# Optimization experiments

Hardware: AMD Instinct MI355X
Metric: run time of the kernel (lower is better)

## Reference

```python
import jax, jax.numpy as jnp
import numpy as np

T, N, E, B = 6, 3200, 32000, 8
IN, G, TOK, H, NH = 128, 128, 512, 4, 8
HD = TOK // NH
NEG_SLOPE = 0.2  # PyG GATv2Conv default negative_slope
L_GAT, L_TF = 3, 2


def _ln(x, g, b, eps=1e-5):
    mu = x.mean(-1, keepdims=True)
    var = ((x - mu) ** 2).mean(-1, keepdims=True)
    return (x - mu) * jax.lax.rsqrt(var + eps) * g + b


def setup_inputs() -> dict:
    key = jax.random.key(0)
    ks = iter(jax.random.split(key, 64))
    nrm = lambda shape, s=0.05: (jax.random.normal(next(ks), shape) * s).astype(jnp.float32)
    return dict(
        x=jax.random.normal(next(ks), (T, N, IN), jnp.float32),
        edge_index=jax.random.randint(next(ks), (T, 2, E), 0, N, dtype=jnp.int32),
        edge_attr=jax.random.normal(next(ks), (T, E, 2), jnp.float32),
        batch=jnp.sort(jax.random.randint(next(ks), (N,), 0, B, dtype=jnp.int32)),
        proj_w=nrm((IN, G)), proj_b=jnp.zeros((G,), jnp.float32),
        gat_wl=nrm((L_GAT, G, H * G)), gat_bl=jnp.zeros((L_GAT, H * G), jnp.float32),
        gat_wr=nrm((L_GAT, G, H * G)), gat_br=jnp.zeros((L_GAT, H * G), jnp.float32),
        gat_we=nrm((L_GAT, 2, H * G)),
        gat_att=nrm((L_GAT, H, G)),
        gat_bias=jnp.zeros((L_GAT, G), jnp.float32),
        ln_g=jnp.ones((L_GAT, G), jnp.float32), ln_b=jnp.zeros((L_GAT, G), jnp.float32),
        n2t_w=nrm((2 * G, TOK)), n2t_b=jnp.zeros((TOK,), jnp.float32),
        tf_wqkv=nrm((L_TF, TOK, 3 * TOK)), tf_bqkv=jnp.zeros((L_TF, 3 * TOK), jnp.float32),
        tf_wo=nrm((L_TF, TOK, TOK)), tf_bo=jnp.zeros((L_TF, TOK), jnp.float32),
        tf_w1=nrm((L_TF, TOK, 4 * TOK)), tf_b1=jnp.zeros((L_TF, 4 * TOK), jnp.float32),
        tf_w2=nrm((L_TF, 4 * TOK, TOK)), tf_b2=jnp.zeros((L_TF, TOK), jnp.float32),
        tf_ln1g=jnp.ones((L_TF, TOK), jnp.float32), tf_ln1b=jnp.zeros((L_TF, TOK), jnp.float32),
        tf_ln2g=jnp.ones((L_TF, TOK), jnp.float32), tf_ln2b=jnp.zeros((L_TF, TOK), jnp.float32),
    )


def reference(x, edge_index, edge_attr, batch,
              proj_w, proj_b,
              gat_wl, gat_bl, gat_wr, gat_br, gat_we, gat_att, gat_bias,
              ln_g, ln_b, n2t_w, n2t_b,
              tf_wqkv, tf_bqkv, tf_wo, tf_bo, tf_w1, tf_b1, tf_w2, tf_b2,
              tf_ln1g, tf_ln1b, tf_ln2g, tf_ln2b):

    def gat(h, src, dst, ea, wl, bl, wr, br, we, att, bias):
        # GATv2Conv: lin_l -> source features (x_j), lin_r -> target (x_i)
        xl = (h @ wl + bl).reshape(N, H, G)
        xr = (h @ wr + br).reshape(N, H, G)
        ee = (ea @ we).reshape(E, H, G)
        m = jax.nn.leaky_relu(xl[src] + xr[dst] + ee, NEG_SLOPE)  # [E,H,G]
        logit = jnp.einsum('ehc,hc->eh', m, att)
        lmax = jax.ops.segment_max(logit, dst, num_segments=N)  # segment softmax over dst
        p = jnp.exp(logit - lmax[dst])
        denom = jax.ops.segment_sum(p, dst, num_segments=N) + 1e-16
        alpha = p / denom[dst]  # [E,H]
        out = jax.ops.segment_sum(xl[src] * alpha[:, :, None], dst, num_segments=N)
        return out.mean(1) + bias  # concat=False -> head mean, [N,G]

    counts = jnp.maximum(
        jax.ops.segment_sum(jnp.ones((N,), x.dtype), batch, num_segments=B), 1.0)

    def per_graph(xg, ei, ea):
        src, dst = ei[0], ei[1]
        h = xg @ proj_w + proj_b
        for l in range(L_GAT):
            out = jax.nn.relu(gat(h, src, dst, ea, gat_wl[l], gat_bl[l],
                                  gat_wr[l], gat_br[l], gat_we[l],
                                  gat_att[l], gat_bias[l]))
            h = _ln(out + h, ln_g[l], ln_b[l])
        mean = jax.ops.segment_sum(h, batch, num_segments=B) / counts[:, None]
        mx = jax.ops.segment_max(h, batch, num_segments=B)
        return jnp.concatenate([mean, mx], -1) @ n2t_w + n2t_b  # [B,TOK]

    tokens = jax.vmap(per_graph)(x, edge_index, edge_attr)  # [T,B,TOK]
    app = tokens.transpose(1, 0, 2)  # [B,T,TOK]
    mot = app[:, 1:] - app[:, :-1]

    h = app
    for l in range(L_TF):  # PyTorch TransformerEncoderLayer, post-norm, relu
        qkv = h @ tf_wqkv[l] + tf_bqkv[l]
        q, k, v = jnp.split(qkv, 3, axis=-1)
        q = q.reshape(B, T, NH, HD)
        k = k.reshape(B, T, NH, HD)
        v = v.reshape(B, T, NH, HD)
        a = jax.nn.softmax(jnp.einsum('bqhd,bkhd->bhqk', q, k) / np.float32(np.sqrt(HD)), -1)
        att_out = jnp.einsum('bhqk,bkhd->bqhd', a, v).reshape(B, T, TOK) @ tf_wo[l] + tf_bo[l]
        h = _ln(h + att_out, tf_ln1g[l], tf_ln1b[l])
        ff = jax.nn.relu(h @ tf_w1[l] + tf_b1[l]) @ tf_w2[l] + tf_b2[l]
        h = _ln(h + ff, tf_ln2g[l], tf_ln2b[l])

    return (h, mot[..., :256])
```

## Files before the change

### kernel.cpp

```cpp
#include <hip/hip_runtime.h>
#include <float.h>
#include <math.h>

#define TT 6
#define NN 3200
#define EE 32000
#define BB 8
#define GF 128
#define TOKF 512
#define NHH 8
#define PCH 16

typedef __attribute__((ext_vector_type(4))) float f32x4;
typedef __attribute__((ext_vector_type(8))) short short8;

static __device__ __forceinline__ float leaky(float v){ return fmaxf(v, 0.2f*v); }
static __device__ __forceinline__ ushort f2bf(float f) {
  uint u = __float_as_uint(f);
  uint r = (u + 0x7fffu + ((u >> 16) & 1u)) >> 16;
  return (ushort)r;
}
static __device__ __forceinline__ float bf2f(uint bits) {
  return __uint_as_float(bits << 16);
}
static __device__ __forceinline__ float bflo(uint u){ return __uint_as_float(u << 16); }
static __device__ __forceinline__ float bfhi(uint u){ return __uint_as_float(u & 0xffff0000u); }

__global__ __launch_bounds__(256) void gemm_tiled(
    const float* __restrict__ A, int lda,
    const float* __restrict__ W, int ldw,
    const float* __restrict__ bias,
    float* __restrict__ C, int ldc,
    int M, int N, int K)
{
  __shared__ float As[64][36];
  __shared__ float Bs[32][64];
  int tid = threadIdx.x;
  int tx = tid & 15, ty = tid >> 4;
  int m0 = blockIdx.y * 64, n0 = blockIdx.x * 64;
  float acc[4][4] = {};
  for (int k0 = 0; k0 < K; k0 += 32) {
    #pragma unroll
    for (int i = 0; i < 2; ++i) {
      int q = tid + i * 256;
      int r = q >> 3, k = (q & 7) * 4;
      *(float4*)&As[r][k] = *(const float4*)&A[(size_t)(m0 + r) * lda + k0 + k];
    }
    #pragma unroll
    for (int i = 0; i < 2; ++i) {
      int q = tid + i * 256;
      int kk = q >> 4, c = (q & 15) * 4;
      *(float4*)&Bs[kk][c] = *(const float4*)&W[(size_t)(k0 + kk) * ldw + n0 + c];
    }
    __syncthreads();
    #pragma unroll
    for (int kk = 0; kk < 32; ++kk) {
      float4 b4 = *(const float4*)&Bs[kk][tx * 4];
      float a0 = As[ty*4+0][kk];
      float a1 = As[ty*4+1][kk];
      float a2 = As[ty*4+2][kk];
      float a3 = As[ty*4+3][kk];
      acc[0][0] += a0*b4.x; acc[0][1] += a0*b4.y; acc[0][2] += a0*b4.z; acc[0][3] += a0*b4.w;
      acc[1][0] += a1*b4.x; acc[1][1] += a1*b4.y; acc[1][2] += a1*b4.z; acc[1][3] += a1*b4.w;
      acc[2][0] += a2*b4.x; acc[2][1] += a2*b4.y; acc[2][2] += a2*b4.z; acc[2][3] += a2*b4.w;
      acc[3][0] += a3*b4.x; acc[3][1] += a3*b4.y; acc[3][2] += a3*b4.z; acc[3][3] += a3*b4.w;
    }
    __syncthreads();
  }
  float4 bia = *(const float4*)&bias[n0 + tx * 4];
  #pragma unroll
  for (int i = 0; i < 4; ++i) {
    float4 v = { acc[i][0] + bia.x, acc[i][1] + bia.y, acc[i][2] + bia.z, acc[i][3] + bia.w };
    *(float4*)&C[(size_t)(m0 + ty*4 + i) * ldc + n0 + tx * 4] = v;
  }
}

__global__ void k_wprep3(const float* __restrict__ gat_wl, const float* __restrict__ gat_wr,
                         ushort* __restrict__ Wt3)
{
  int gid = blockIdx.x * 256 + threadIdx.x;
  if (gid >= 3 * 1024 * 128) return;
  int l = gid >> 17;
  int rem = gid & (1024 * 128 - 1);
  int n = rem >> 7, k = rem & 127;
  const float* wl = gat_wl + (size_t)l * 128 * 512;
  const float* wr = gat_wr + (size_t)l * 128 * 512;
  float v = (n < 512) ? wl[(size_t)k * 512 + n] : wr[(size_t)k * 512 + (n - 512)];
  Wt3[gid] = f2bf(v);
}

__global__ __launch_bounds__(256) void gat_lr_gemm_mfma(
    const float* __restrict__ A,
    const ushort* __restrict__ Wt,
    const float* __restrict__ bl, const float* __restrict__ br,
    ushort* __restrict__ C)
{
  __shared__ ushort Asm[64 * 128];
  __shared__ ushort Wsm[64 * 128];
  int tid = threadIdx.x;
  int m0 = blockIdx.y * 64, n0 = blockIdx.x * 64;

  #pragma unroll
  for (int i = 0; i < 4; ++i) {
    int g = tid + i * 256;
    int row = g >> 4, gk = g & 15;
    const float* src = A + (size_t)(m0 + row) * 128 + gk * 8;
    float4 f0 = *(const float4*)src;
    float4 f1 = *(const float4*)(src + 4);
    short8 hv;
    hv[0] = (short)f2bf(f0.x); hv[1] = (short)f2bf(f0.y);
    hv[2] = (short)f2bf(f0.z); hv[3] = (short)f2bf(f0.w);
    hv[4] = (short)f2bf(f1.x); hv[5] = (short)f2bf(f1.y);
    hv[6] = (short)f2bf(f1.z); hv[7] = (short)f2bf(f1.w);
    *(short8*)&Asm[row * 128 + (gk ^ (row & 7)) * 8] = hv;
  }
  #pragma unroll
  for (int i = 0; i < 4; ++i) {
    int g = tid + i * 256;
    int col = g >> 4, gk = g & 15;
    short8 raw = *(const short8*)&Wt[(size_t)(n0 + col) * 128 + gk * 8];
    *(short8*)&Wsm[col * 128 + (gk ^ (col & 7)) * 8] = raw;
  }
  __syncthreads();

  int l = tid & 63, wv = tid >> 6;
  int wr_ = wv >> 1, wc_ = wv & 1;
  int lr = l & 15, lk = l >> 4;
  f32x4 acc[2][2] = {};
  #pragma unroll
  for (int ks = 0; ks < 4; ++ks) {
    int g = ks * 4 + lk;
    int ra0 = wr_ * 32 + lr,      ra1 = wr_ * 32 + 16 + lr;
    int rb0 = wc_ * 32 + lr,      rb1 = wc_ * 32 + 16 + lr;
    short8 a0 = *(short8*)&Asm[ra0 * 128 + (g ^ (ra0 & 7)) * 8];
    short8 a1 = *(short8*)&Asm[ra1 * 128 + (g ^ (ra1 & 7)) * 8];
    short8 b0 = *(short8*)&Wsm[rb0 * 128 + (g ^ (rb0 & 7)) * 8];
    short8 b1 = *(short8*)&Wsm[rb1 * 128 + (g ^ (rb1 & 7)) * 8];
    acc[0][0] = __builtin_amdgcn_mfma_f32_16x16x32_bf16(a0, b0, acc[0][0], 0, 0, 0);
    acc[0][1] = __builtin_amdgcn_mfma_f32_16x16x32_bf16(a0, b1, acc[0][1], 0, 0, 0);
    acc[1][0] = __builtin_amdgcn_mfma_f32_16x16x32_bf16(a1, b0, acc[1][0], 0, 0, 0);
    acc[1][1] = __builtin_amdgcn_mfma_f32_16x16x32_bf16(a1, b1, acc[1][1], 0, 0, 0);
  }

  int col_l = l & 15, row_l = (l >> 4) * 4;
  #pragma unroll
  for (int fn = 0; fn < 2; ++fn) {
    int n_g = n0 + wc_ * 32 + fn * 16 + col_l;
    float bia = (n_g < 512) ? bl[n_g] : br[n_g - 512];
    #pragma unroll
    for (int fm = 0; fm < 2; ++fm) {
      #pragma unroll
      for (int r = 0; r < 4; ++r) {
        int m = m0 + wr_ * 32 + fm * 16 + row_l + r;
        C[(size_t)m * 1024 + n_g] = f2bf(acc[fm][fn][r] + bia);
      }
    }
  }
}

__global__ __launch_bounds__(256) void gemm_part(
    const float* __restrict__ A, int lda,
    const float* __restrict__ W, int ldw,
    float* __restrict__ P, int N)
{
  __shared__ float As[48][132];
  __shared__ float Ws[128][32];
  int tid = threadIdx.x;
  int n0 = blockIdx.x * 32, k0 = blockIdx.y * 128;
  #pragma unroll
  for (int i = 0; i < 6; ++i) {
    int q = tid + i * 256;
    int m = q >> 5, k = (q & 31) * 4;
    *(float4*)&As[m][k] = *(const float4*)&A[(size_t)m * lda + k0 + k];
  }
  #pragma unroll
  for (int i = 0; i < 4; ++i) {
    int q = tid + i * 256;
    int k = q >> 3, c = (q & 7) * 4;
    *(float4*)&Ws[k][c] = *(const float4*)&W[(size_t)(k0 + k) * ldw + n0 + c];
  }
  __syncthreads();
  int tx = tid & 31, ty = tid >> 5;
  float acc[6] = {};
  #pragma unroll 4
  for (int k = 0; k < 128; ++k) {
    float w = Ws[k][tx];
    #pragma unroll
    for (int i = 0; i < 6; ++i) acc[i] += As[ty + 8*i][k] * w;
  }
  size_t base = (size_t)blockIdx.y * 48 * N;
  #pragma unroll
  for (int i = 0; i < 6; ++i)
    P[base + (size_t)(ty + 8*i) * N + n0 + tx] = acc[i];
}

__global__ void k_part_reduce(const float* __restrict__ P, const float* __restrict__ bias,
                              float* __restrict__ C, int MN, int N, int nparts, int relu)
{
  int i = blockIdx.x * 256 + threadIdx.x;
  if (i >= MN) return;
  float s = bias[i % N];
  for (int p = 0; p < nparts; ++p) s += P[(size_t)p * MN + i];
  C[i] = relu ? fmaxf(s, 0.f) : s;
}

__global__ void k_n2t_reduce(const float* __restrict__ P, const float* __restrict__ bias,
                             float* __restrict__ happ)
{
  int i = blockIdx.x * 256 + threadIdx.x;
  if (i >= 48 * 512) return;
  int j = i & 511, r = i >> 9;
  int t = r >> 3, b = r & 7;
  float s = bias[j];
  #pragma unroll
  for (int p = 0; p < 2; ++p) s += P[(size_t)p * 48 * 512 + i];
  happ[((size_t)(b * TT) + t) * 512 + j] = s;
}

__global__ void k_hist(const int* __restrict__ edge_index, int* __restrict__ cnt)
{
  int gid = blockIdx.x * 256 + threadIdx.x;
  if (gid >= TT * EE) return;
  int t = gid / EE, e = gid - t * EE;
  int dst = edge_index[t * 2 * EE + EE + e];
  atomicAdd(&cnt[t * NN + dst], 1);
}

__global__ __launch_bounds__(256) void k_scan(const int* __restrict__ cnt, int* __restrict__ row)
{
  __shared__ int part[256];
  int t = blockIdx.x, tid = threadIdx.x;
  const int chunk = (NN + 255) / 256;
  int s0 = tid * chunk;
  int loc = 0;
  for (int i = 0; i < chunk; ++i) { int idx = s0 + i; if (idx < NN) loc += cnt[t*NN + idx]; }
  part[tid] = loc; __syncthreads();
  for (int off = 1; off < 256; off <<= 1) {
    int v = (tid >= off) ? part[tid - off] : 0;
    __syncthreads();
    part[tid] += v;
    __syncthreads();
  }
  int run = part[tid] - loc;
  for (int i = 0; i < chunk; ++i) {
    int idx = s0 + i;
    if (idx < NN) { row[t*(NN+1) + idx] = run; run += cnt[t*NN + idx]; }
  }
  if (tid == 255) row[t*(NN+1) + NN] = part[255];
}

__global__ void k_scatter(const int* __restrict__ edge_index, const float* __restrict__ ea,
                          const int* __restrict__ row, int* __restrict__ cur,
                          int* __restrict__ srcs, float2* __restrict__ ea_csr)
{
  int gid = blockIdx.x * 256 + threadIdx.x;
  if (gid >= TT * EE) return;
  int t = gid / EE, e = gid - t * EE;
  int src = edge_index[t * 2 * EE + e];
  int dst = edge_index[t * 2 * EE + EE + e];
  float2 ev = *(const float2*)&ea[((size_t)t * EE + e) * 2];
  int pos = row[t*(NN+1) + dst] + atomicAdd(&cur[t*NN + dst], 1);
  int s = t * EE + pos;
  srcs[s] = src;
  ea_csr[s] = ev;
}

__global__ void k_gstart(const int* __restrict__ batch, int* __restrict__ gs)
{
  int n = blockIdx.x * 256 + threadIdx.x;
  if (n >= NN) return;
  int bc = batch[n];
  if (n == 0) { for (int j = 0; j <= bc; ++j) gs[j] = 0; }
  else { int bp = batch[n-1]; for (int j = bp + 1; j <= bc; ++j) gs[j] = n; }
  if (n == NN - 1) { for (int j = bc + 1; j <= BB; ++j) gs[j] = NN; }
}

__global__ __launch_bounds__(256) void k_gat_fused1w(
    const ushort* __restrict__ xlr, const int* __restrict__ row,
    const int* __restrict__ srcs, const float2* __restrict__ ea_csr,
    const float* __restrict__ we, const float* __restrict__ att,
    const float* __restrict__ bias,
    const float* __restrict__ lng, const float* __restrict__ lnb,
    const float* __restrict__ h_in, float* __restrict__ h_out)
{
  int wv = threadIdx.x >> 6, l = threadIdx.x & 63;
  int t = blockIdx.y;
  int n = blockIdx.x * 4 + wv;
  int hd = l >> 4, q = l & 15;
  int ub = hd * 64 + q * 4;
  float2 w0[4], w1[4], at4[4];
  #pragma unroll
  for (int j = 0; j < 4; ++j) {
    int j0 = (ub + j) * 2;
    w0[j]  = make_float2(we[j0],        we[j0 + 1]);
    w1[j]  = make_float2(we[512 + j0],  we[512 + j0 + 1]);
    at4[j] = make_float2(att[j0],       att[j0 + 1]);
  }
  int start = row[t * (NN + 1) + n];
  int end   = row[t * (NN + 1) + n + 1];

  const uint* xd = (const uint*)(xlr + ((size_t)t * NN + n) * 1024 + 512);
  uint4 ud = *(const uint4*)&xd[ub];
  float xrv[8];
  xrv[0] = bflo(ud.x); xrv[1] = bfhi(ud.x);
  xrv[2] = bflo(ud.y); xrv[3] = bfhi(ud.y);
  xrv[4] = bflo(ud.z); xrv[5] = bfhi(ud.z);
  xrv[6] = bflo(ud.w); xrv[7] = bfhi(ud.w);

  size_t sb = (size_t)t * EE;
  const ushort* xbase = xlr + (size_t)t * NN * 1024;

  float ssum = 0.f;
  float acc[8] = {};

  auto edge_proc = [&](uint4 us, float2 eav) {
    float xv[8];
    xv[0] = bflo(us.x); xv[1] = bfhi(us.x);
    xv[2] = bflo(us.y); xv[3] = bfhi(us.y);
    xv[4] = bflo(us.z); xv[5] = bfhi(us.z);
    xv[6] = bflo(us.w); xv[7] = bfhi(us.w);
    float lg = 0.f;
    #pragma unroll
    for (int j = 0; j < 4; ++j) {
      float lo = xv[2*j] + xrv[2*j];
      lo = fmaf(eav.x, w0[j].x, lo);
      lo = fmaf(eav.y, w1[j].x, lo);
      lg = fmaf(leaky(lo), at4[j].x, lg);
      float hi = xv[2*j+1] + xrv[2*j+1];
      hi = fmaf(eav.x, w0[j].y, hi);
      hi = fmaf(eav.y, w1[j].y, hi);
      lg = fmaf(leaky(hi), at4[j].y, lg);
    }
    lg += __shfl_xor(lg, 1, 64);
    lg += __shfl_xor(lg, 2, 64);
    lg += __shfl_xor(lg, 4, 64);
    lg += __shfl_xor(lg, 8, 64);
    float w = __expf(fminf(lg, 60.f));
    ssum += w;
    #pragma unroll
    for (int j = 0; j < 8; ++j) acc[j] = fmaf(w, xv[j], acc[j]);
  };

  int p = start;
  for (; p + 4 <= end; p += 4) {
    int sA = srcs[sb + p],     sB = srcs[sb + p + 1];
    int sC = srcs[sb + p + 2], sD = srcs[sb + p + 3];
    float2 eA = ea_csr[sb + p],     eB = ea_csr[sb + p + 1];
    float2 eC = ea_csr[sb + p + 2], eD = ea_csr[sb + p + 3];
    uint4 uA = *(const uint4*)&((const uint*)(xbase + (size_t)sA * 1024))[ub];
    uint4 uB = *(const uint4*)&((const uint*)(xbase + (size_t)sB * 1024))[ub];
    uint4 uC = *(const uint4*)&((const uint*)(xbase + (size_t)sC * 1024))[ub];
    uint4 uD = *(const uint4*)&((const uint*)(xbase + (size_t)sD * 1024))[ub];
    edge_proc(uA, eA);
    edge_proc(uB, eB);
    edge_proc(uC, eC);
    edge_proc(uD, eD);
  }
  for (; p < end; ++p) {
    int sA = srcs[sb + p];
    float2 eA = ea_csr[sb + p];
    uint4 uA = *(const uint4*)&((const uint*)(xbase + (size_t)sA * 1024))[ub];
    edge_proc(uA, eA);
  }

  float inv = 1.f / (ssum + 1e-16f);
  #pragma unroll
  for (int j = 0; j < 8; ++j) acc[j] *= inv;

  #pragma unroll
  for (int j = 0; j < 8; ++j) {
    float v = acc[j];
    v += __shfl_xor(v, 16, 64);
    v += __shfl_xor(v, 32, 64);
    acc[j] = v * 0.25f;
  }

  const float* hin = h_in + ((size_t)t * NN + n) * 128 + q * 8;
  float4 hi0 = *(const float4*)hin;
  float4 hi1 = *(const float4*)(hin + 4);
  float4 bi0 = *(const float4*)&bias[q * 8];
  float4 bi1 = *(const float4*)&bias[q * 8 + 4];
  float val[8];
  val[0] = fmaxf(acc[0] + bi0.x, 0.f) + hi0.x;
  val[1] = fmaxf(acc[1] + bi0.y, 0.f) + hi0.y;
  val[2] = fmaxf(acc[2] + bi0.z, 0.f) + hi0.z;
  val[3] = fmaxf(acc[3] + bi0.w, 0.f) + hi0.w;
  val[4] = fmaxf(acc[4] + bi1.x, 0.f) + hi1.x;
  val[5] = fmaxf(acc[5] + bi1.y, 0.f) + hi1.y;
  val[6] = fmaxf(acc[6] + bi1.z, 0.f) + hi1.z;
  val[7] = fmaxf(acc[7] + bi1.w, 0.f) + hi1.w;

  float s1 = 0.f, s2 = 0.f;
  #pragma unroll
  for (int j = 0; j < 8; ++j) { s1 += val[j]; s2 += val[j] * val[j]; }
  #pragma unroll
  for (int o = 1; o < 16; o <<= 1) {
    s1 += __shfl_xor(s1, o, 64);
    s2 += __shfl_xor(s2, o, 64);
  }
  float mu = s1 * (1.f / 128.f);
  float var = fmaxf(s2 * (1.f / 128.f) - mu * mu, 0.f);
  float rstd = rsqrtf(var + 1e-5f);
  if (hd == 0) {
    float4 g0 = *(const float4*)&lng[q * 8];
    float4 g1 = *(const float4*)&lng[q * 8 + 4];
    float4 b0 = *(const float4*)&lnb[q * 8];
    float4 b1 = *(const float4*)&lnb[q * 8 + 4];
    float4 o0, o1;
    o0.x = (val[0] - mu) * rstd * g0.x + b0.x;
    o0.y = (val[1] - mu) * rstd * g0.y + b0.y;
    o0.z = (val[2] - mu) * rstd * g0.z + b0.z;
    o0.w = (val[3] - mu) * rstd * g0.w + b0.w;
    o1.x = (val[4] - mu) * rstd * g1.x + b1.x;
    o1.y = (val[5] - mu) * rstd * g1.y + b1.y;
    o1.z = (val[6] - mu) * rstd * g1.z + b1.z;
    o1.w = (val[7] - mu) * rstd * g1.w + b1.w;
    float* hout = h_out + ((size_t)t * NN + n) * 128 + q * 8;
    *(float4*)hout = o0;
    *(float4*)(hout + 4) = o1;
  }
}

__global__ __launch_bounds__(128) void k_pool1(
    const float* __restrict__ h, const int* __restrict__ gs, float* __restrict__ part)
{
  int b = blockIdx.x, t = blockIdx.y, ch = blockIdx.z, c = threadIdx.x;
  int s0 = gs[b], s1 = gs[b + 1];
  int len = s1 - s0;
  int per = (len + PCH - 1) / PCH;
  int a0 = s0 + ch * per;
  int a1 = min(a0 + per, s1);
  float sum = 0.f, mx = -FLT_MAX;
  for (int n = a0; n < a1; ++n) {
    float v = h[((size_t)t * NN + n) * 128 + c];
    sum += v; mx = fmaxf(mx, v);
  }
  size_t o = (((size_t)(t * BB + b) * PCH + ch) * 2) * 128 + c;
  part[o] = sum; part[o + 128] = mx;
}

__global__ __launch_bounds__(128) void k_pool2(
    const float* __restrict__ part, const int* __restrict__ gs, float* __restrict__ pooled)
{
  int b = blockIdx.x, t = blockIdx.y, c = threadIdx.x;
  float sum = 0.f, mx = -FLT_MAX;
  for (int ch = 0; ch < PCH; ++ch) {
    size_t o = (((size_t)(t * BB + b) * PCH + ch) * 2) * 128 + c;
    sum += part[o]; mx = fmaxf(mx, part[o + 128]);
  }
  int cnt = gs[b + 1] - gs[b]; if (cnt < 1) cnt = 1;
  pooled[((size_t)t * BB + b) * 256 + c] = sum / (float)cnt;
  pooled[((size_t)t * BB + b) * 256 + 128 + c] = mx;
}

__global__ void k_mot(const float* __restrict__ happ, float* __restrict__ out2)
{
  int gid = blockIdx.x * 256 + threadIdx.x;
  if (gid >= BB * (TT - 1) * 256) return;
  int b = gid / ((TT - 1) * 256);
  int r = gid - b * ((TT - 1) * 256);
  int ti = r / 256, cc = r - ti * 256;
  out2[gid] = happ[((size_t)(b * TT) + ti + 1) * 512 + cc]
            - happ[((size_t)(b * TT) + ti) * 512 + cc];
}

__global__ __launch_bounds__(64) void k_attn(const float* __restrict__ P,
                                             const float* __restrict__ bias,
                                             float* __restrict__ aout)
{
  __shared__ float qs[TT][64], ks[TT][64], vs[TT][64], sc[TT][TT];
  int h = blockIdx.x, b = blockIdx.y, d = threadIdx.x;
  const int MN = 48 * 1536;
  float bq = bias[h * 64 + d], bk = bias[512 + h * 64 + d], bv = bias[1024 + h * 64 + d];
  for (int i = 0; i < TT; ++i) {
    size_t base = ((size_t)(b * TT + i)) * 1536 + h * 64 + d;
    float q = bq, k = bk, v = bv;
    #pragma unroll
    for (int p = 0; p < 4; ++p) {
      q += P[(size_t)p * MN + base];
      k += P[(size_t)p * MN + base + 512];
      v += P[(size_t)p * MN + base + 1024];
    }
    qs[i][d] = q; ks[i][d] = k; vs[i][d] = v;
  }
  __syncthreads();
  if (d < TT * TT) {
    int i = d / TT, j = d - i * TT;
    float s = 0.f;
    for (int k = 0; k < 64; ++k) s += qs[i][k] * ks[j][k];
    sc[i][j] = s * 0.125f;
  }
  __syncthreads();
  if (d < TT) {
    float mx = -FLT_MAX;
    for (int j = 0; j < TT; ++j) mx = fmaxf(mx, sc[d][j]);
    float sum = 0.f;
    for (int j = 0; j < TT; ++j) { float e = expf(sc[d][j] - mx); sc[d][j] = e; sum += e; }
    float inv = 1.f / sum;
    for (int j = 0; j < TT; ++j) sc[d][j] *= inv;
  }
  __syncthreads();
  for (int i = 0; i < TT; ++i) {
    float o = 0.f;
    for (int j = 0; j < TT; ++j) o += sc[i][j] * vs[j][d];
    aout[((size_t)(b * TT + i)) * 512 + h * 64 + d] = o;
  }
}

__global__ __launch_bounds__(256) void k_res_ln_p(
    const float* __restrict__ P, int nparts, const float* __restrict__ bias,
    const float* __restrict__ r,
    const float* __restrict__ g, const float* __restrict__ be,
    float* __restrict__ out)
{
  __shared__ float2 wred[4];
  int rowi = blockIdx.x, tid = threadIdx.x;
  size_t base = (size_t)rowi * 512;
  const int MN = 48 * 512;
  float v0 = bias[tid], v1 = bias[256 + tid];
  for (int p = 0; p < nparts; ++p) {
    v0 += P[(size_t)p * MN + base + tid];
    v1 += P[(size_t)p * MN + base + 256 + tid];
  }
  v0 += r[base + tid];
  v1 += r[base + 256 + tid];
  float s1 = v0 + v1, s2 = v0 * v0 + v1 * v1;
  #pragma unroll
  for (int o = 32; o > 0; o >>= 1) {
    s1 += __shfl_xor(s1, o, 64);
    s2 += __shfl_xor(s2, o, 64);
  }
  int wv = tid >> 6, l = tid & 63;
  if (l == 0) wred[wv] = make_float2(s1, s2);
  __syncthreads();
  float t1 = wred[0].x + wred[1].x + wred[2].x + wred[3].x;
  float t2 = wred[0].y + wred[1].y + wred[2].y + wred[3].y;
  float mu = t1 * (1.f / 512.f);
  float var = fmaxf(t2 * (1.f / 512.f) - mu * mu, 0.f);
  float rstd = rsqrtf(var + 1e-5f);
  out[base + tid]       = (v0 - mu) * rstd * g[tid]       + be[tid];
  out[base + 256 + tid] = (v1 - mu) * rstd * g[256 + tid] + be[256 + tid];
}

extern "C" void kernel_launch(void* const* d_in, const int* in_sizes, int n_in,
                              void* d_out, int out_size, void* d_ws, size_t ws_size,
                              hipStream_t stream)
{
  const float* x        = (const float*)d_in[0];
  const int*   eidx     = (const int*)  d_in[1];
  const float* eattr    = (const float*)d_in[2];
  const int*   batch    = (const int*)  d_in[3];
  const float* proj_w   = (const float*)d_in[4];
  const float* proj_b   = (const float*)d_in[5];
  const float* gat_wl   = (const float*)d_in[6];
  const float* gat_bl   = (const float*)d_in[7];
  const float* gat_wr   = (const float*)d_in[8];
  const float* gat_br   = (const float*)d_in[9];
  const float* gat_we   = (const float*)d_in[10];
  const float* gat_att  = (const float*)d_in[11];
  const float* gat_bias = (const float*)d_in[12];
  const float* ln_g     = (const float*)d_in[13];
  const float* ln_b     = (const float*)d_in[14];
  const float* n2t_w    = (const float*)d_in[15];
  const float* n2t_b    = (const float*)d_in[16];
  const float* tf_wqkv  = (const float*)d_in[17];
  const float* tf_bqkv  = (const float*)d_in[18];
  const float* tf_wo    = (const float*)d_in[19];
  const float* tf_bo    = (const float*)d_in[20];
  const float* tf_w1    = (const float*)d_in[21];
  const float* tf_b1    = (const float*)d_in[22];
  const float* tf_w2    = (const float*)d_in[23];
  const float* tf_b2    = (const float*)d_in[24];
  const float* tf_ln1g  = (const float*)d_in[25];
  const float* tf_ln1b  = (const float*)d_in[26];
  const float* tf_ln2g  = (const float*)d_in[27];
  const float* tf_ln2b  = (const float*)d_in[28];

  char* ws = (char*)d_ws;
  size_t off = 0;
  auto alloc = [&](size_t bytes) -> char* {
    char* p = ws + off;
    off += (bytes + 255) & ~(size_t)255;
    return p;
  };
  int*    cnt    = (int*)   alloc((size_t)TT * NN * 4);
  int*    row    = (int*)   alloc((size_t)TT * (NN + 1) * 4);
  int*    srcs   = (int*)   alloc((size_t)TT * EE * 4);
  float2* ea_csr = (float2*)alloc((size_t)TT * EE * 8);
  int*    gs     = (int*)   alloc((BB + 1) * 4);
  float*  h0     = (float*) alloc((size_t)TT * NN * 128 * 4);
  float*  h1     = (float*) alloc((size_t)TT * NN * 128 * 4);
  ushort* xlr    = (ushort*)alloc((size_t)TT * NN * 1024 * 2);
  ushort* Wt3    = (ushort*)alloc((size_t)3 * 1024 * 128 * 2);
  float*  part   = (float*) alloc((size_t)TT * BB * PCH * 2 * 128 * 4);
  float*  pooled = (float*) alloc((size_t)TT * BB * 256 * 4);
  float*  happ   = (float*) alloc((size_t)BB * TT * 512 * 4);
  float*  happ2  = (float*) alloc((size_t)BB * TT * 512 * 4);
  float*  aoutb  = (float*) alloc((size_t)BB * TT * 512 * 4);
  float*  ffb    = (float*) alloc((size_t)BB * TT * 2048 * 4);
  if (off > ws_size) return;

  float* P = (float*)xlr;

  hipMemsetAsync(cnt, 0, (size_t)TT * NN * 4, stream);
  k_hist<<<(TT * EE + 255) / 256, 256, 0, stream>>>(eidx, cnt);
  k_scan<<<TT, 256, 0, stream>>>(cnt, row);
  hipMemsetAsync(cnt, 0, (size_t)TT * NN * 4, stream);
  k_scatter<<<(TT * EE + 255) / 256, 256, 0, stream>>>(eidx, eattr, row, cnt, srcs, ea_csr);
  k_gstart<<<(NN + 255) / 256, 256, 0, stream>>>(batch, gs);

  k_wprep3<<<(3 * 1024 * 128 + 255) / 256, 256, 0, stream>>>(gat_wl, gat_wr, Wt3);
  gemm_tiled<<<dim3(2, (TT * NN) / 64), 256, 0, stream>>>(
      x, 128, proj_w, 128, proj_b, h0, 128, TT * NN, 128, 128);

  float* hcur = h0; float* hnext = h1;
  for (int l = 0; l < 3; ++l) {
    const float* bl  = gat_bl  + (size_t)l * 512;
    const float* br  = gat_br  + (size_t)l * 512;
    const float* we  = gat_we  + (size_t)l * 2 * 512;
    const float* att = gat_att + (size_t)l * 512;
    gat_lr_gemm_mfma<<<dim3(16, 300), 256, 0, stream>>>(hcur, Wt3 + (size_t)l * 1024 * 128, bl, br, xlr);
    k_gat_fused1w<<<dim3(NN / 4, TT), 256, 0, stream>>>(xlr, row, srcs, ea_csr, we, att,
        gat_bias + l * 128, ln_g + l * 128, ln_b + l * 128, hcur, hnext);
    float* tmp = hcur; hcur = hnext; hnext = tmp;
  }

  k_pool1<<<dim3(BB, TT, PCH), 128, 0, stream>>>(hcur, gs, part);
  k_pool2<<<dim3(BB, TT), 128, 0, stream>>>(part, gs, pooled);
  gemm_part<<<dim3(512 / 32, 2), 256, 0, stream>>>(pooled, 256, n2t_w, 512, P, 512);
  k_n2t_reduce<<<(48 * 512 + 255) / 256, 256, 0, stream>>>(P, n2t_b, happ);
  k_mot<<<(BB * (TT - 1) * 256 + 255) / 256, 256, 0, stream>>>(happ, (float*)d_out + BB * TT * TOKF);

  float* hx = happ;
  for (int l = 0; l < 2; ++l) {
    gemm_part<<<dim3(1536 / 32, 4), 256, 0, stream>>>(hx, 512,
        tf_wqkv + (size_t)l * 512 * 1536, 1536, P, 1536);
    k_attn<<<dim3(NHH, BB), 64, 0, stream>>>(P, tf_bqkv + l * 1536, aoutb);
    gemm_part<<<dim3(512 / 32, 4), 256, 0, stream>>>(aoutb, 512,
        tf_wo + (size_t)l * 512 * 512, 512, P, 512);
    k_res_ln_p<<<BB * TT, 256, 0, stream>>>(P, 4, tf_bo + l * 512, hx,
        tf_ln1g + l * 512, tf_ln1b + l * 512, happ2);
    gemm_part<<<dim3(2048 / 32, 4), 256, 0, stream>>>(happ2, 512,
        tf_w1 + (size_t)l * 512 * 2048, 2048, P, 2048);
    k_part_reduce<<<(48 * 2048 + 255) / 256, 256, 0, stream>>>(P, tf_b1 + l * 2048, ffb, 48 * 2048, 2048, 4, 1);
    gemm_part<<<dim3(512 / 32, 16), 256, 0, stream>>>(ffb, 2048,
        tf_w2 + (size_t)l * 2048 * 512, 512, P, 512);
    float* dst = (l == 1) ? (float*)d_out : happ;
    k_res_ln_p<<<BB * TT, 256, 0, stream>>>(P, 16, tf_b2 + l * 512, happ2,
        tf_ln2g + l * 512, tf_ln2b + l * 512, dst);
    hx = happ;
  }
}
```

Measured before the change: 355.6 us.

## Pack CSR edge data into int4 and loop GAT nodes grid-stride

Merges the separate CSR source-index and edge-attribute arrays into one 16-byte int4 record per edge, so each edge needs a single vector load. The fused GAT aggregation kernel becomes a grid-stride loop over nodes with half as many blocks (400 per timestep), so the per-lane weight and attention constants loaded at kernel start are reused across two nodes. The per-edge arithmetic is rewritten with float2 helpers. The int4 record adds 4 bytes of padding per edge, and the smaller grid may reduce latency hiding for the gather loads.

```diff
diff --git a/kernel.cpp b/kernel.cpp
--- a/kernel.cpp
+++ b/kernel.cpp
@@ -25,6 +25,11 @@
 }
 static __device__ __forceinline__ float bflo(uint u){ return __uint_as_float(u << 16); }
 static __device__ __forceinline__ float bfhi(uint u){ return __uint_as_float(u & 0xffff0000u); }
+
+static __device__ __forceinline__ float2 add2(float2 a, float2 b){ return make_float2(a.x+b.x, a.y+b.y); }
+static __device__ __forceinline__ float2 fma2s(float s, float2 b, float2 c){ return make_float2(fmaf(s,b.x,c.x), fmaf(s,b.y,c.y)); }
+static __device__ __forceinline__ float2 fma2v(float2 a, float2 b, float2 c){ return make_float2(fmaf(a.x,b.x,c.x), fmaf(a.y,b.y,c.y)); }
+static __device__ __forceinline__ float2 leaky2(float2 v){ return make_float2(fmaxf(v.x, 0.2f*v.x), fmaxf(v.y, 0.2f*v.y)); }
 
 __global__ __launch_bounds__(256) void gemm_tiled(
     const float* __restrict__ A, int lda,
@@ -251,7 +256,7 @@
 
 __global__ void k_scatter(const int* __restrict__ edge_index, const float* __restrict__ ea,
                           const int* __restrict__ row, int* __restrict__ cur,
-                          int* __restrict__ srcs, float2* __restrict__ ea_csr)
+                          int4* __restrict__ edg)
 {
   int gid = blockIdx.x * 256 + threadIdx.x;
   if (gid >= TT * EE) return;
@@ -261,8 +266,7 @@
   float2 ev = *(const float2*)&ea[((size_t)t * EE + e) * 2];
   int pos = row[t*(NN+1) + dst] + atomicAdd(&cur[t*NN + dst], 1);
   int s = t * EE + pos;
-  srcs[s] = src;
-  ea_csr[s] = ev;
+  edg[s] = make_int4(src, __float_as_int(ev.x), __float_as_int(ev.y), 0);
 }
 
 __global__ void k_gstart(const int* __restrict__ batch, int* __restrict__ gs)
@@ -277,7 +281,7 @@
 
 __global__ __launch_bounds__(256) void k_gat_fused1w(
     const ushort* __restrict__ xlr, const int* __restrict__ row,
-    const int* __restrict__ srcs, const float2* __restrict__ ea_csr,
+    const int4* __restrict__ edg,
     const float* __restrict__ we, const float* __restrict__ att,
     const float* __restrict__ bias,
     const float* __restrict__ lng, const float* __restrict__ lnb,
@@ -285,7 +289,6 @@
 {
   int wv = threadIdx.x >> 6, l = threadIdx.x & 63;
   int t = blockIdx.y;
-  int n = blockIdx.x * 4 + wv;
   int hd = l >> 4, q = l & 15;
   int ub = hd * 64 + q * 4;
   float2 w0[4], w1[4], at4[4];
@@ -296,128 +299,127 @@
     w1[j]  = make_float2(we[512 + j0],  we[512 + j0 + 1]);
     at4[j] = make_float2(att[j0],       att[j0 + 1]);
   }
-  int start = row[t * (NN + 1) + n];
-  int end   = row[t * (NN + 1) + n + 1];
-
-  const uint* xd = (const uint*)(xlr + ((size_t)t * NN + n) * 1024 + 512);
-  uint4 ud = *(const uint4*)&xd[ub];
-  float xrv[8];
-  xrv[0] = bflo(ud.x); xrv[1] = bfhi(ud.x);
-  xrv[2] = bflo(ud.y); xrv[3] = bfhi(ud.y);
-  xrv[4] = bflo(ud.z); xrv[5] = bfhi(ud.z);
-  xrv[6] = bflo(ud.w); xrv[7] = bfhi(ud.w);
-
   size_t sb = (size_t)t * EE;
   const ushort* xbase = xlr + (size_t)t * NN * 1024;
-
-  float ssum = 0.f;
-  float acc[8] = {};
-
-  auto edge_proc = [&](uint4 us, float2 eav) {
-    float xv[8];
-    xv[0] = bflo(us.x); xv[1] = bfhi(us.x);
-    xv[2] = bflo(us.y); xv[3] = bfhi(us.y);
-    xv[4] = bflo(us.z); xv[5] = bfhi(us.z);
-    xv[6] = bflo(us.w); xv[7] = bfhi(us.w);
-    float lg = 0.f;
+  int nstride = gridDim.x * 4;
+
+  for (int n = blockIdx.x * 4 + wv; n < NN; n += nstride) {
+    int start = row[t * (NN + 1) + n];
+    int end   = row[t * (NN + 1) + n + 1];
+
+    const uint* xd = (const uint*)(xbase + (size_t)n * 1024 + 512);
+    uint4 udv = *(const uint4*)&xd[ub];
+    float2 xrv[4];
+    xrv[0] = make_float2(bflo(udv.x), bfhi(udv.x));
+    xrv[1] = make_float2(bflo(udv.y), bfhi(udv.y));
+    xrv[2] = make_float2(bflo(udv.z), bfhi(udv.z));
+    xrv[3] = make_float2(bflo(udv.w), bfhi(udv.w));
+
+    float ssum = 0.f;
+    float2 acc[4] = {};
+
+    auto edge_proc = [&](uint4 us, float e0, float e1) {
+      float2 xv[4];
+      xv[0] = make_float2(bflo(us.x), bfhi(us.x));
+      xv[1] = make_float2(bflo(us.y), bfhi(us.y));
+      xv[2] = make_float2(bflo(us.z), bfhi(us.z));
+      xv[3] = make_float2(bflo(us.w), bfhi(us.w));
+      float2 lg2 = make_float2(0.f, 0.f);
+      #pragma unroll
+      for (int j = 0; j < 4; ++j) {
+        float2 s = add2(xv[j], xrv[j]);
+        s = fma2s(e0, w0[j], s);
+        s = fma2s(e1, w1[j], s);
+        lg2 = fma2v(leaky2(s), at4[j], lg2);
+      }
+      float lg = lg2.x + lg2.y;
+      lg += __shfl_xor(lg, 1, 64);
+      lg += __shfl_xor(lg, 2, 64);
+      lg += __shfl_xor(lg, 4, 64);
+      lg += __shfl_xor(lg, 8, 64);
+      float w = __expf(fminf(lg, 60.f));
+      ssum += w;
+      #pragma unroll
+      for (int j = 0; j < 4; ++j) acc[j] = fma2s(w, xv[j], acc[j]);
+    };
+
+    int p = start;
+    for (; p + 4 <= end; p += 4) {
+      int4 eA = edg[sb + p],     eB = edg[sb + p + 1];
+      int4 eC = edg[sb + p + 2], eD = edg[sb + p + 3];
+      uint4 uA = *(const uint4*)&((const uint*)(xbase + (size_t)eA.x * 1024))[ub];
+      uint4 uB = *(const uint4*)&((const uint*)(xbase + (size_t)eB.x * 1024))[ub];
+      uint4 uC = *(const uint4*)&((const uint*)(xbase + (size_t)eC.x * 1024))[ub];
+      uint4 uD = *(const uint4*)&((const uint*)(xbase + (size_t)eD.x * 1024))[ub];
+      edge_proc(uA, __int_as_float(eA.y), __int_as_float(eA.z));
+      edge_proc(uB, __int_as_float(eB.y), __int_as_float(eB.z));
+      edge_proc(uC, __int_as_float(eC.y), __int_as_float(eC.z));
+      edge_proc(uD, __int_as_float(eD.y), __int_as_float(eD.z));
+    }
+    for (; p < end; ++p) {
+      int4 eA = edg[sb + p];
+      uint4 uA = *(const uint4*)&((const uint*)(xbase + (size_t)eA.x * 1024))[ub];
+      edge_proc(uA, __int_as_float(eA.y), __int_as_float(eA.z));
+    }
+
+    float inv = 1.f / (ssum + 1e-16f);
+    #pragma unroll
+    for (int j = 0; j < 4; ++j) { acc[j].x *= inv; acc[j].y *= inv; }
+
     #pragma unroll
     for (int j = 0; j < 4; ++j) {
-      float lo = xv[2*j] + xrv[2*j];
-      lo = fmaf(eav.x, w0[j].x, lo);
-      lo = fmaf(eav.y, w1[j].x, lo);
-      lg = fmaf(leaky(lo), at4[j].x, lg);
-      float hi = xv[2*j+1] + xrv[2*j+1];
-      hi = fmaf(eav.x, w0[j].y, hi);
-      hi = fmaf(eav.y, w1[j].y, hi);
-      lg = fmaf(leaky(hi), at4[j].y, lg);
-    }
-    lg += __shfl_xor(lg, 1, 64);
-    lg += __shfl_xor(lg, 2, 64);
-    lg += __shfl_xor(lg, 4, 64);
-    lg += __shfl_xor(lg, 8, 64);
-    float w = __expf(fminf(lg, 60.f));
-    ssum += w;
-    #pragma unroll
-    for (int j = 0; j < 8; ++j) acc[j] = fmaf(w, xv[j], acc[j]);
-  };
-
-  int p = start;
-  for (; p + 4 <= end; p += 4) {
-    int sA = srcs[sb + p],     sB = srcs[sb + p + 1];
-    int sC = srcs[sb + p + 2], sD = srcs[sb + p + 3];
-    float2 eA = ea_csr[sb + p],     eB = ea_csr[sb + p + 1];
-    float2 eC = ea_csr[sb + p + 2], eD = ea_csr[sb + p + 3];
-    uint4 uA = *(const uint4*)&((const uint*)(xbase + (size_t)sA * 1024))[ub];
-    uint4 uB = *(const uint4*)&((const uint*)(xbase + (size_t)sB * 1024))[ub];
-    uint4 uC = *(const uint4*)&((const uint*)(xbase + (size_t)sC * 1024))[ub];
-    uint4 uD = *(const uint4*)&((const uint*)(xbase + (size_t)sD * 1024))[ub];
-    edge_proc(uA, eA);
-    edge_proc(uB, eB);
-    edge_proc(uC, eC);
-    edge_proc(uD, eD);
-  }
-  for (; p < end; ++p) {
-    int sA = srcs[sb + p];
-    float2 eA = ea_csr[sb + p];
-    uint4 uA = *(const uint4*)&((const uint*)(xbase + (size_t)sA * 1024))[ub];
-    edge_proc(uA, eA);
-  }
-
-  float inv = 1.f / (ssum + 1e-16f);
-  #pragma unroll
-  for (int j = 0; j < 8; ++j) acc[j] *= inv;
-
-  #pragma unroll
-  for (int j = 0; j < 8; ++j) {
-    float v = acc[j];
-    v += __shfl_xor(v, 16, 64);
-    v += __shfl_xor(v, 32, 64);
-    acc[j] = v * 0.25f;
-  }
-
-  const float* hin = h_in + ((size_t)t * NN + n) * 128 + q * 8;
-  float4 hi0 = *(const float4*)hin;
-  float4 hi1 = *(const float4*)(hin + 4);
-  float4 bi0 = *(const float4*)&bias[q * 8];
-  float4 bi1 = *(const float4*)&bias[q * 8 + 4];
-  float val[8];
-  val[0] = fmaxf(acc[0] + bi0.x, 0.f) + hi0.x;
-  val[1] = fmaxf(acc[1] + bi0.y, 0.f) + hi0.y;
-  val[2] = fmaxf(acc[2] + bi0.z, 0.f) + hi0.z;
-  val[3] = fmaxf(acc[3] + bi0.w, 0.f) + hi0.w;
-  val[4] = fmaxf(acc[4] + bi1.x, 0.f) + hi1.x;
-  val[5] = fmaxf(acc[5] + bi1.y, 0.f) + hi1.y;
-  val[6] = fmaxf(acc[6] + bi1.z, 0.f) + hi1.z;
-  val[7] = fmaxf(acc[7] + bi1.w, 0.f) + hi1.w;
-
-  float s1 = 0.f, s2 = 0.f;
-  #pragma unroll
-  for (int j = 0; j < 8; ++j) { s1 += val[j]; s2 += val[j] * val[j]; }
-  #pragma unroll
-  for (int o = 1; o < 16; o <<= 1) {
-    s1 += __shfl_xor(s1, o, 64);
-    s2 += __shfl_xor(s2, o, 64);
-  }
-  float mu = s1 * (1.f / 128.f);
-  float var = fmaxf(s2 * (1.f / 128.f) - mu * mu, 0.f);
-  float rstd = rsqrtf(var + 1e-5f);
-  if (hd == 0) {
-    float4 g0 = *(const float4*)&lng[q * 8];
-    float4 g1 = *(const float4*)&lng[q * 8 + 4];
-    float4 b0 = *(const float4*)&lnb[q * 8];
-    float4 b1 = *(const float4*)&lnb[q * 8 + 4];
-    float4 o0, o1;
-    o0.x = (val[0] - mu) * rstd * g0.x + b0.x;
-    o0.y = (val[1] - mu) * rstd * g0.y + b0.y;
-    o0.z = (val[2] - mu) * rstd * g0.z + b0.z;
-    o0.w = (val[3] - mu) * rstd * g0.w + b0.w;
-    o1.x = (val[4] - mu) * rstd * g1.x + b1.x;
-    o1.y = (val[5] - mu) * rstd * g1.y + b1.y;
-    o1.z = (val[6] - mu) * rstd * g1.z + b1.z;
-    o1.w = (val[7] - mu) * rstd * g1.w + b1.w;
-    float* hout = h_out + ((size_t)t * NN + n) * 128 + q * 8;
-    *(float4*)hout = o0;
-    *(float4*)(hout + 4) = o1;
+      float vx = acc[j].x, vy = acc[j].y;
+      vx += __shfl_xor(vx, 16, 64);
+      vx += __shfl_xor(vx, 32, 64);
+      vy += __shfl_xor(vy, 16, 64);
+      vy += __shfl_xor(vy, 32, 64);
+      acc[j] = make_float2(vx * 0.25f, vy * 0.25f);
+    }
+
+    const float* hin = h_in + ((size_t)t * NN + n) * 128 + q * 8;
+    float4 hi0 = *(const float4*)hin;
+    float4 hi1 = *(const float4*)(hin + 4);
+    float4 bi0 = *(const float4*)&bias[q * 8];
+    float4 bi1 = *(const float4*)&bias[q * 8 + 4];
+    float val[8];
+    val[0] = fmaxf(acc[0].x + bi0.x, 0.f) + hi0.x;
+    val[1] = fmaxf(acc[0].y + bi0.y, 0.f) + hi0.y;
+    val[2] = fmaxf(acc[1].x + bi0.z, 0.f) + hi0.z;
+    val[3] = fmaxf(acc[1].y + bi0.w, 0.f) + hi0.w;
+    val[4] = fmaxf(acc[2].x + bi1.x, 0.f) + hi1.x;
+    val[5] = fmaxf(acc[2].y + bi1.y, 0.f) + hi1.y;
+    val[6] = fmaxf(acc[3].x + bi1.z, 0.f) + hi1.z;
+    val[7] = fmaxf(acc[3].y + bi1.w, 0.f) + hi1.w;
+
+    float s1 = 0.f, s2 = 0.f;
+    #pragma unroll
+    for (int j = 0; j < 8; ++j) { s1 += val[j]; s2 += val[j] * val[j]; }
+    #pragma unroll
+    for (int o = 1; o < 16; o <<= 1) {
+      s1 += __shfl_xor(s1, o, 64);
+      s2 += __shfl_xor(s2, o, 64);
+    }
+    float mu = s1 * (1.f / 128.f);
+    float var = fmaxf(s2 * (1.f / 128.f) - mu * mu, 0.f);
+    float rstd = rsqrtf(var + 1e-5f);
+    if (hd == 0) {
+      float4 g0 = *(const float4*)&lng[q * 8];
+      float4 g1 = *(const float4*)&lng[q * 8 + 4];
+      float4 b0 = *(const float4*)&lnb[q * 8];
+      float4 b1 = *(const float4*)&lnb[q * 8 + 4];
+      float4 o0, o1;
+      o0.x = (val[0] - mu) * rstd * g0.x + b0.x;
+      o0.y = (val[1] - mu) * rstd * g0.y + b0.y;
+      o0.z = (val[2] - mu) * rstd * g0.z + b0.z;
+      o0.w = (val[3] - mu) * rstd * g0.w + b0.w;
+      o1.x = (val[4] - mu) * rstd * g1.x + b1.x;
+      o1.y = (val[5] - mu) * rstd * g1.y + b1.y;
+      o1.z = (val[6] - mu) * rstd * g1.z + b1.z;
+      o1.w = (val[7] - mu) * rstd * g1.w + b1.w;
+      float* hout = h_out + ((size_t)t * NN + n) * 128 + q * 8;
+      *(float4*)hout = o0;
+      *(float4*)(hout + 4) = o1;
+    }
   }
 }
 
@@ -585,8 +587,7 @@
   };
   int*    cnt    = (int*)   alloc((size_t)TT * NN * 4);
   int*    row    = (int*)   alloc((size_t)TT * (NN + 1) * 4);
-  int*    srcs   = (int*)   alloc((size_t)TT * EE * 4);
-  float2* ea_csr = (float2*)alloc((size_t)TT * EE * 8);
+  int4*   edg    = (int4*)  alloc((size_t)TT * EE * 16);
   int*    gs     = (int*)   alloc((BB + 1) * 4);
   float*  h0     = (float*) alloc((size_t)TT * NN * 128 * 4);
   float*  h1     = (float*) alloc((size_t)TT * NN * 128 * 4);
@@ -606,7 +607,7 @@
   k_hist<<<(TT * EE + 255) / 256, 256, 0, stream>>>(eidx, cnt);
   k_scan<<<TT, 256, 0, stream>>>(cnt, row);
   hipMemsetAsync(cnt, 0, (size_t)TT * NN * 4, stream);
-  k_scatter<<<(TT * EE + 255) / 256, 256, 0, stream>>>(eidx, eattr, row, cnt, srcs, ea_csr);
+  k_scatter<<<(TT * EE + 255) / 256, 256, 0, stream>>>(eidx, eattr, row, cnt, edg);
   k_gstart<<<(NN + 255) / 256, 256, 0, stream>>>(batch, gs);
 
   k_wprep3<<<(3 * 1024 * 128 + 255) / 256, 256, 0, stream>>>(gat_wl, gat_wr, Wt3);
@@ -620,7 +621,7 @@
     const float* we  = gat_we  + (size_t)l * 2 * 512;
     const float* att = gat_att + (size_t)l * 512;
     gat_lr_gemm_mfma<<<dim3(16, 300), 256, 0, stream>>>(hcur, Wt3 + (size_t)l * 1024 * 128, bl, br, xlr);
-    k_gat_fused1w<<<dim3(NN / 4, TT), 256, 0, stream>>>(xlr, row, srcs, ea_csr, we, att,
+    k_gat_fused1w<<<dim3(400, TT), 256, 0, stream>>>(xlr, row, edg, we, att,
         gat_bias + l * 128, ln_g + l * 128, ln_b + l * 128, hcur, hnext);
     float* tmp = hcur; hcur = hnext; hnext = tmp;
   }
```

Result: slower. 374.6 us (+5.4%).

## Split GAT edge aggregation across two waves per node and fuse FFN partial reduce

Applied to the files above, without the earlier changes.

The GAT aggregation kernel now assigns two waves to each destination node. Each wave processes half of the node's incoming edges, and the two partial sums and softmax denominators are combined through shared memory. This doubles the number of blocks and halves the serial edge loop per wave, aiming for more memory-level parallelism on the gather. Separately, the FFN split-K reduce plus bias and ReLU is folded into the A-tile load of the second FFN GEMM, which removes one launch and the ffb round trip. In exchange the fused GEMM rereads the four partials once per output-column block, and it writes to a new P2 buffer so it does not overwrite the partials it is still reading.

```diff
diff --git a/kernel.cpp b/kernel.cpp
--- a/kernel.cpp
+++ b/kernel.cpp
@@ -19,9 +19,6 @@
   uint u = __float_as_uint(f);
   uint r = (u + 0x7fffu + ((u >> 16) & 1u)) >> 16;
   return (ushort)r;
-}
-static __device__ __forceinline__ float bf2f(uint bits) {
-  return __uint_as_float(bits << 16);
 }
 static __device__ __forceinline__ float bflo(uint u){ return __uint_as_float(u << 16); }
 static __device__ __forceinline__ float bfhi(uint u){ return __uint_as_float(u & 0xffff0000u); }
@@ -194,14 +191,49 @@
     P[base + (size_t)(ty + 8*i) * N + n0 + tx] = acc[i];
 }
 
-__global__ void k_part_reduce(const float* __restrict__ P, const float* __restrict__ bias,
-                              float* __restrict__ C, int MN, int N, int nparts, int relu)
-{
-  int i = blockIdx.x * 256 + threadIdx.x;
-  if (i >= MN) return;
-  float s = bias[i % N];
-  for (int p = 0; p < nparts; ++p) s += P[(size_t)p * MN + i];
-  C[i] = relu ? fmaxf(s, 0.f) : s;
+__global__ __launch_bounds__(256) void gemm_part_pr(
+    const float* __restrict__ Pin, int npartsA, const float* __restrict__ biasA,
+    const float* __restrict__ W, int ldw,
+    float* __restrict__ P, int N)
+{
+  __shared__ float As[48][132];
+  __shared__ float Ws[128][32];
+  int tid = threadIdx.x;
+  int n0 = blockIdx.x * 32, k0 = blockIdx.y * 128;
+  const int MNA = 48 * 2048;
+  #pragma unroll
+  for (int i = 0; i < 6; ++i) {
+    int q = tid + i * 256;
+    int m = q >> 5, k = (q & 31) * 4;
+    size_t base = (size_t)m * 2048 + k0 + k;
+    float4 s = *(const float4*)&biasA[k0 + k];
+    for (int p = 0; p < 4; ++p) {
+      float4 v = *(const float4*)&Pin[(size_t)p * MNA + base];
+      s.x += v.x; s.y += v.y; s.z += v.z; s.w += v.w;
+    }
+    s.x = fmaxf(s.x, 0.f); s.y = fmaxf(s.y, 0.f);
+    s.z = fmaxf(s.z, 0.f); s.w = fmaxf(s.w, 0.f);
+    *(float4*)&As[m][k] = s;
+  }
+  #pragma unroll
+  for (int i = 0; i < 4; ++i) {
+    int q = tid + i * 256;
+    int k = q >> 3, c = (q & 7) * 4;
+    *(float4*)&Ws[k][c] = *(const float4*)&W[(size_t)(k0 + k) * ldw + n0 + c];
+  }
+  __syncthreads();
+  int tx = tid & 31, ty = tid >> 5;
+  float acc[6] = {};
+  #pragma unroll 4
+  for (int k = 0; k < 128; ++k) {
+    float w = Ws[k][tx];
+    #pragma unroll
+    for (int i = 0; i < 6; ++i) acc[i] += As[ty + 8*i][k] * w;
+  }
+  size_t base = (size_t)blockIdx.y * 48 * N;
+  #pragma unroll
+  for (int i = 0; i < 6; ++i)
+    P[base + (size_t)(ty + 8*i) * N + n0 + tx] = acc[i];
 }
 
 __global__ void k_n2t_reduce(const float* __restrict__ P, const float* __restrict__ bias,
@@ -283,9 +315,11 @@
     const float* __restrict__ lng, const float* __restrict__ lnb,
     const float* __restrict__ h_in, float* __restrict__ h_out)
 {
+  __shared__ float sacc[4][64][9];
   int wv = threadIdx.x >> 6, l = threadIdx.x & 63;
   int t = blockIdx.y;
-  int n = blockIdx.x * 4 + wv;
+  int n = blockIdx.x * 2 + (wv >> 1);
+  int half = wv & 1;
   int hd = l >> 4, q = l & 15;
   int ub = hd * 64 + q * 4;
   float2 w0[4], w1[4], at4[4];
@@ -296,8 +330,12 @@
     w1[j]  = make_float2(we[512 + j0],  we[512 + j0 + 1]);
     at4[j] = make_float2(att[j0],       att[j0 + 1]);
   }
-  int start = row[t * (NN + 1) + n];
-  int end   = row[t * (NN + 1) + n + 1];
+  int seg0 = row[t * (NN + 1) + n];
+  int seg1 = row[t * (NN + 1) + n + 1];
+  int len  = seg1 - seg0;
+  int h0len = (len + 1) >> 1;
+  int start = half ? seg0 + h0len : seg0;
+  int end   = half ? seg1 : seg0 + h0len;
 
   const uint* xd = (const uint*)(xlr + ((size_t)t * NN + n) * 1024 + 512);
   uint4 ud = *(const uint4*)&xd[ub];
@@ -362,6 +400,15 @@
     uint4 uA = *(const uint4*)&((const uint*)(xbase + (size_t)sA * 1024))[ub];
     edge_proc(uA, eA);
   }
+
+  #pragma unroll
+  for (int j = 0; j < 8; ++j) sacc[wv][l][j] = acc[j];
+  sacc[wv][l][8] = ssum;
+  __syncthreads();
+  if (half) return;
+  #pragma unroll
+  for (int j = 0; j < 8; ++j) acc[j] += sacc[wv + 1][l][j];
+  ssum += sacc[wv + 1][l][8];
 
   float inv = 1.f / (ssum + 1e-16f);
   #pragma unroll
@@ -597,7 +644,7 @@
   float*  happ   = (float*) alloc((size_t)BB * TT * 512 * 4);
   float*  happ2  = (float*) alloc((size_t)BB * TT * 512 * 4);
   float*  aoutb  = (float*) alloc((size_t)BB * TT * 512 * 4);
-  float*  ffb    = (float*) alloc((size_t)BB * TT * 2048 * 4);
+  float*  P2     = (float*) alloc((size_t)16 * 48 * 512 * 4);
   if (off > ws_size) return;
 
   float* P = (float*)xlr;
@@ -620,7 +667,7 @@
     const float* we  = gat_we  + (size_t)l * 2 * 512;
     const float* att = gat_att + (size_t)l * 512;
     gat_lr_gemm_mfma<<<dim3(16, 300), 256, 0, stream>>>(hcur, Wt3 + (size_t)l * 1024 * 128, bl, br, xlr);
-    k_gat_fused1w<<<dim3(NN / 4, TT), 256, 0, stream>>>(xlr, row, srcs, ea_csr, we, att,
+    k_gat_fused1w<<<dim3(NN / 2, TT), 256, 0, stream>>>(xlr, row, srcs, ea_csr, we, att,
         gat_bias + l * 128, ln_g + l * 128, ln_b + l * 128, hcur, hnext);
     float* tmp = hcur; hcur = hnext; hnext = tmp;
   }
@@ -642,11 +689,10 @@
         tf_ln1g + l * 512, tf_ln1b + l * 512, happ2);
     gemm_part<<<dim3(2048 / 32, 4), 256, 0, stream>>>(happ2, 512,
         tf_w1 + (size_t)l * 512 * 2048, 2048, P, 2048);
-    k_part_reduce<<<(48 * 2048 + 255) / 256, 256, 0, stream>>>(P, tf_b1 + l * 2048, ffb, 48 * 2048, 2048, 4, 1);
-    gemm_part<<<dim3(512 / 32, 16), 256, 0, stream>>>(ffb, 2048,
-        tf_w2 + (size_t)l * 2048 * 512, 512, P, 512);
+    gemm_part_pr<<<dim3(512 / 32, 16), 256, 0, stream>>>(P, 4, tf_b1 + l * 2048,
+        tf_w2 + (size_t)l * 2048 * 512, 512, P2, 512);
     float* dst = (l == 1) ? (float*)d_out : happ;
-    k_res_ln_p<<<BB * TT, 256, 0, stream>>>(P, 16, tf_b2 + l * 512, happ2,
+    k_res_ln_p<<<BB * TT, 256, 0, stream>>>(P2, 16, tf_b2 + l * 512, happ2,
         tf_ln2g + l * 512, tf_ln2b + l * 512, dst);
     hx = happ;
   }
```

Measured after the change: 373.4 us. +5.0%, slower.
